# Optimization experiments

Hardware: AMD Instinct MI355X
Metric: run time of the kernel (lower is better)

Reference implementation:

```python
import jax, jax.numpy as jnp
import numpy as np

N = 50000
E = 800000
D = 128


def setup_inputs() -> dict:
    key = jax.random.key(0)
    ks = jax.random.split(key, 10)
    x = jax.random.normal(ks[0], (N, D), dtype=jnp.float32)
    edge_index = jax.random.randint(ks[1], (2, E), 0, N, dtype=jnp.int32)
    s = 1.0 / np.sqrt(D)
    W1 = jax.random.uniform(ks[2], (D, D), jnp.float32, -s, s)
    b1 = jnp.zeros((D,), jnp.float32)
    W2 = jax.random.uniform(ks[3], (D, D), jnp.float32, -s, s)
    b2 = jnp.zeros((D,), jnp.float32)
    Wt = jax.random.uniform(ks[4], (D, 1), jnp.float32, -s, s)
    bt = jnp.zeros((1,), jnp.float32)
    We = jax.random.uniform(ks[5], (D, 1), jnp.float32, -s, s)
    be = jnp.zeros((1,), jnp.float32)
    return {"x": x, "edge_index": edge_index, "W1": W1, "b1": b1,
            "W2": W2, "b2": b2, "Wt": Wt, "bt": bt, "We": We, "be": be}


def _gcn_norm(edge_index, n):
    # add self-loops, then symmetric normalization D^-1/2 (A+I) D^-1/2
    loop = jnp.arange(n, dtype=edge_index.dtype)
    src = jnp.concatenate([edge_index[0], loop])
    dst = jnp.concatenate([edge_index[1], loop])
    ones = jnp.ones(src.shape[0], dtype=jnp.float32)
    deg = jax.ops.segment_sum(ones, dst, num_segments=n)
    dinv = jnp.where(deg > 0, jax.lax.rsqrt(deg), 0.0)
    norm = dinv[src] * dinv[dst]  # [E+N]
    return src, dst, norm


def _gcn_conv(h, W, b, src, dst, norm, n):
    h = h @ W                                   # [N, D'] dense GEMM
    msg = h[src] * norm[:, None]                # gather + scale
    out = jax.ops.segment_sum(msg, dst, num_segments=n)  # scatter-add
    return out + b


def reference(x, edge_index, W1, b1, W2, b2, Wt, bt, We, be):
    n = x.shape[0]
    src, dst, norm = _gcn_norm(edge_index, n)
    h = jax.nn.relu(_gcn_conv(x, W1, b1, src, dst, norm, n))
    h = jax.nn.relu(_gcn_conv(h, W2, b2, src, dst, norm, n))
    # dropout is identity at inference (eval mode)
    survival_time = h @ Wt + bt   # [N, 1]
    event_status = h @ We + be    # [N, 1]
    return survival_time, event_status
```

## Files before the change

kernel.cpp:

```cpp
#include <hip/hip_runtime.h>
#include <hip/hip_fp16.h>
#include <math.h>

#define NN 50000
#define NE 800000
#define DD 128

#define NB  196
#define CAP 5300
#define EPB 4096

#define CONV_B 6250

typedef _Float16 half8_t __attribute__((ext_vector_type(8)));
typedef float f32x4 __attribute__((ext_vector_type(4)));


__global__ __launch_bounds__(256) void k_init_bcur(int* __restrict__ bcur) {
    int t = threadIdx.x;
    if (t < NB) bcur[t] = t * CAP;
}

__global__ __launch_bounds__(256) void k_phaseA(const int* __restrict__ src, const int* __restrict__ dst,
                                                int* __restrict__ bcur, unsigned int* __restrict__ ebuf) {
    __shared__ int hist[256];
    __shared__ int scanbuf[256];
    __shared__ int gbase[256];
    __shared__ unsigned int stage[EPB];
    __shared__ int tgt[EPB];

    const int tid = threadIdx.x;
    const int e0  = blockIdx.x * EPB;
    int nE = NE - e0; if (nE > EPB) nE = EPB;

    hist[tid] = 0;
    __syncthreads();

    unsigned int pk[16];
    unsigned int br[16];
    #pragma unroll
    for (int j = 0; j < 16; ++j) {
        int idx = tid + j * 256;
        if (idx < nE) {
            int e = e0 + idx;
            int s = src[e], d = dst[e];
            int b = d >> 8;
            int r = atomicAdd(&hist[b], 1);
            pk[j] = (unsigned int)s | ((unsigned int)(d & 255) << 16);
            br[j] = (unsigned int)b | ((unsigned int)r << 8);
        }
    }
    __syncthreads();
    int v = hist[tid];
    scanbuf[tid] = v;
    __syncthreads();
    for (int o = 1; o < 256; o <<= 1) {
        int t2 = (tid >= o) ? scanbuf[tid - o] : 0;
        __syncthreads();
        scanbuf[tid] += t2;
        __syncthreads();
    }
    int base_excl = scanbuf[tid] - v;
    if (tid < NB && v > 0) gbase[tid] = atomicAdd(&bcur[tid], v);
    hist[tid] = base_excl;
    __syncthreads();

    #pragma unroll
    for (int j = 0; j < 16; ++j) {
        int idx = tid + j * 256;
        if (idx < nE) {
            int b = br[j] & 255;
            int r = (int)(br[j] >> 8);
            int pos = hist[b] + r;
            stage[pos] = pk[j];
            tgt[pos]   = gbase[b] + r;
        }
    }
    __syncthreads();
    #pragma unroll
    for (int j = 0; j < 16; ++j) {
        int idx = tid + j * 256;
        if (idx < nE) ebuf[tgt[idx]] = stage[idx];
    }
}

__global__ __launch_bounds__(256) void k_bucket_scan(const int* __restrict__ bcur, int* __restrict__ bbase,
                                                     int* __restrict__ row_ptr) {
    __shared__ int s[256];
    int tid = threadIdx.x;
    int sz = (tid < NB) ? (bcur[tid] - tid * CAP) : 0;
    s[tid] = sz;
    __syncthreads();
    for (int o = 1; o < 256; o <<= 1) {
        int t = (tid >= o) ? s[tid - o] : 0;
        __syncthreads();
        s[tid] += t;
        __syncthreads();
    }
    if (tid < NB) bbase[tid] = s[tid] - sz;
    if (tid == 0) row_ptr[NN] = NE;
}

__global__ __launch_bounds__(256) void k_build_csr(const unsigned int* __restrict__ ebuf,
                                                   const int* __restrict__ bcur,
                                                   const int* __restrict__ bbase,
                                                   int* __restrict__ row_ptr,
                                                   float* __restrict__ dinv,
                                                   unsigned short* __restrict__ col) {
    __shared__ int cnt[256];
    __shared__ int scanb[256];
    __shared__ unsigned short stage[CAP];

    const int b   = blockIdx.x;
    const int tid = threadIdx.x;
    const int seg0 = b * CAP;
    const int sb   = bcur[b] - seg0;
    const int n0   = b << 8;
    int nb = NN - n0; if (nb > 256) nb = 256;

    cnt[tid] = 0;
    __syncthreads();
    for (int p = tid; p < sb; p += 256) {
        unsigned int e = ebuf[seg0 + p];
        atomicAdd(&cnt[(e >> 16) & 255], 1);
    }
    __syncthreads();
    int v = cnt[tid];
    scanb[tid] = v;
    __syncthreads();
    for (int o = 1; o < 256; o <<= 1) {
        int t = (tid >= o) ? scanb[tid - o] : 0;
        __syncthreads();
        scanb[tid] += t;
        __syncthreads();
    }
    int excl = scanb[tid] - v;
    const int rbase = bbase[b];
    if (tid < nb) {
        row_ptr[n0 + tid] = rbase + excl;
        dinv[n0 + tid] = rsqrtf(1.0f + (float)v);
    }
    cnt[tid] = excl;
    __syncthreads();
    for (int p = tid; p < sb; p += 256) {
        unsigned int e = ebuf[seg0 + p];
        int pos = atomicAdd(&cnt[(e >> 16) & 255], 1);
        stage[pos] = (unsigned short)(e & 0xFFFFu);
    }
    __syncthreads();
    for (int p = tid; p < sb; p += 256) {
        col[rbase + p] = stage[p];
    }
}


__global__ __launch_bounds__(256) void k_prep(const float* __restrict__ x,
                                              const float* __restrict__ W1, const float* __restrict__ W2,
                                              __half* __restrict__ Xh,
                                              __half* __restrict__ WT1, __half* __restrict__ WT2) {
    int b = blockIdx.x;
    int tid = threadIdx.x;
    if (b < CONV_B) {
        int idx = b * 256 + tid;
        if (idx < (NN * DD) / 4) {
            float4 v = ((const float4*)x)[idx];
            __half2 a = __floats2half2_rn(v.x, v.y);
            __half2 c = __floats2half2_rn(v.z, v.w);
            uint2 pk;
            pk.x = *(unsigned int*)&a;
            pk.y = *(unsigned int*)&c;
            ((uint2*)Xh)[idx] = pk;
        }
    } else {
        const float* W  = (b == CONV_B) ? W1 : W2;
        __half*      WT = (b == CONV_B) ? WT1 : WT2;
        int n = tid >> 1;
        int k0 = (tid & 1) * 64;
        #pragma unroll 8
        for (int j = 0; j < 64; ++j) {
            int k = k0 + j;
            WT[n * DD + k] = __float2half(W[k * DD + n]);
        }
    }
}


#define LPAD 136

__global__ __launch_bounds__(256) void k_gemm_mfma(const __half* __restrict__ Xh, const __half* __restrict__ WT,
                                                   const float* __restrict__ dinv, __half* __restrict__ G) {
    __shared__ __half Wl[DD * LPAD];
    __shared__ __half Al[64 * LPAD];

    const int tid  = threadIdx.x;
    const int row0 = blockIdx.x * 64;

    {
        const uint4* WTg = (const uint4*)WT;
        #pragma unroll
        for (int j = 0; j < 8; ++j) {
            int u = tid + j * 256;
            int n = u >> 4, koff = (u & 15) * 8;
            uint4 v = WTg[u];
            *(uint4*)&Wl[n * LPAD + koff] = v;
        }
    }
    {
        #pragma unroll
        for (int j = 0; j < 4; ++j) {
            int u = tid + j * 256;
            int r = u >> 4, koff = (u & 15) * 8;
            uint4 v;
            if (row0 + r < NN) v = *(const uint4*)&Xh[(size_t)(row0 + r) * DD + koff];
            else { v.x = 0; v.y = 0; v.z = 0; v.w = 0; }
            *(uint4*)&Al[r * LPAD + koff] = v;
        }
    }
    __syncthreads();

    const int wave = tid >> 6;
    const int lane = tid & 63;
    const int m    = lane & 15;
    const int quad = lane >> 4;

    f32x4 acc[8];
    #pragma unroll
    for (int t = 0; t < 8; ++t) acc[t] = (f32x4){0.f, 0.f, 0.f, 0.f};

    #pragma unroll
    for (int kk = 0; kk < DD; kk += 32) {
        half8_t a = *(const half8_t*)&Al[(wave * 16 + m) * LPAD + kk + quad * 8];
        #pragma unroll
        for (int t = 0; t < 8; ++t) {
            half8_t b = *(const half8_t*)&Wl[(t * 16 + m) * LPAD + kk + quad * 8];
            acc[t] = __builtin_amdgcn_mfma_f32_16x16x32_f16(a, b, acc[t], 0, 0, 0);
        }
    }

    __syncthreads();

    float4 dv = *(const float4*)&dinv[row0 + wave * 16 + quad * 4];

    #pragma unroll
    for (int t = 0; t < 8; ++t) {
        #pragma unroll
        for (int r = 0; r < 4; ++r) {
            int row_l = wave * 16 + quad * 4 + r;
            int c     = t * 16 + m;
            float val = acc[t][r] * ((const float*)&dv)[r];
            Al[row_l * LPAD + c] = __float2half(val);
        }
    }
    __syncthreads();

    {
        #pragma unroll
        for (int j = 0; j < 4; ++j) {
            int u = tid + j * 256;
            int r = u >> 4, koff = (u & 15) * 8;
            if (row0 + r < NN) {
                uint4 v = *(const uint4*)&Al[r * LPAD + koff];
                *(uint4*)&G[(size_t)(row0 + r) * DD + koff] = v;
            }
        }
    }
}


__device__ inline float4 h4_to_f4(uint2 r) {
    __half2 a = *(__half2*)&r.x;
    __half2 b = *(__half2*)&r.y;
    float2 lo = __half22float2(a), hi = __half22float2(b);
    return make_float4(lo.x, lo.y, hi.x, hi.y);
}

__device__ inline uint2 f4_to_h4(float4 v) {
    __half2 a = __floats2half2_rn(v.x, v.y);
    __half2 b = __floats2half2_rn(v.z, v.w);
    uint2 r;
    r.x = *(unsigned int*)&a;
    r.y = *(unsigned int*)&b;
    return r;
}

__device__ inline float4 gather_node4(const __half* __restrict__ G, int node, int lane,
                                      const unsigned short* __restrict__ col, int beg, int end) {
    const int hs = lane >> 5;
    const int fo = lane & 31;
    const size_t foff = (size_t)fo * 4;

    float4 accA, accB = make_float4(0.f, 0.f, 0.f, 0.f);
    {
        float4 v = h4_to_f4(*(const uint2*)(G + (size_t)node * DD + foff));
        accA = (hs == 0) ? v : make_float4(0.f, 0.f, 0.f, 0.f);
    }

    int p = beg;
    for (; p + 3 < end; p += 4) {
        int sA = col[p + hs];
        int sB = col[p + 2 + hs];
        float4 vA = h4_to_f4(*(const uint2*)(G + (size_t)sA * DD + foff));
        float4 vB = h4_to_f4(*(const uint2*)(G + (size_t)sB * DD + foff));
        accA.x += vA.x; accA.y += vA.y; accA.z += vA.z; accA.w += vA.w;
        accB.x += vB.x; accB.y += vB.y; accB.z += vB.z; accB.w += vB.w;
    }
    for (; p < end; p += 2) {
        int idx = p + hs;
        bool active = (hs == 0) || (p + 1 < end);
        if (idx >= end) idx = p;
        int s = col[idx];
        float4 v = h4_to_f4(*(const uint2*)(G + (size_t)s * DD + foff));
        if (active) {
            accA.x += v.x; accA.y += v.y; accA.z += v.z; accA.w += v.w;
        }
    }
    accA.x += accB.x; accA.y += accB.y; accA.z += accB.z; accA.w += accB.w;
    accA.x += __shfl_xor(accA.x, 32, 64);
    accA.y += __shfl_xor(accA.y, 32, 64);
    accA.z += __shfl_xor(accA.z, 32, 64);
    accA.w += __shfl_xor(accA.w, 32, 64);
    return accA;
}

__global__ __launch_bounds__(256) void k_aggregate(const __half* __restrict__ G, const float* __restrict__ dinv,
                                                   const int* __restrict__ row_ptr, const unsigned short* __restrict__ col,
                                                   const float* __restrict__ bias, __half* __restrict__ H) {
    int node = blockIdx.x * 4 + (threadIdx.x >> 6);
    if (node >= NN) return;
    int lane = threadIdx.x & 63;

    int beg = row_ptr[node];
    int end = row_ptr[node + 1];
    float4 acc = gather_node4(G, node, lane, col, beg, end);

    float di = dinv[node];
    int fo = lane & 31;
    float4 bv = ((const float4*)bias)[fo];
    float4 hv;
    hv.x = fmaxf(fmaf(di, acc.x, bv.x), 0.f);
    hv.y = fmaxf(fmaf(di, acc.y, bv.y), 0.f);
    hv.z = fmaxf(fmaf(di, acc.z, bv.z), 0.f);
    hv.w = fmaxf(fmaf(di, acc.w, bv.w), 0.f);
    if ((lane >> 5) == 0) {
        *(uint2*)(H + (size_t)node * DD + (size_t)fo * 4) = f4_to_h4(hv);
    }
}

__global__ __launch_bounds__(256) void k_aggregate_heads(const __half* __restrict__ G, const float* __restrict__ dinv,
                                                         const int* __restrict__ row_ptr, const unsigned short* __restrict__ col,
                                                         const float* __restrict__ bias,
                                                         const float* __restrict__ Wt, const float* __restrict__ bt,
                                                         const float* __restrict__ We, const float* __restrict__ be,
                                                         float* __restrict__ out) {
    int node = blockIdx.x * 4 + (threadIdx.x >> 6);
    if (node >= NN) return;
    int lane = threadIdx.x & 63;

    int beg = row_ptr[node];
    int end = row_ptr[node + 1];
    float4 acc = gather_node4(G, node, lane, col, beg, end);

    float di = dinv[node];
    int fo = lane & 31;
    float4 bv = ((const float4*)bias)[fo];
    float hx = fmaxf(fmaf(di, acc.x, bv.x), 0.f);
    float hy = fmaxf(fmaf(di, acc.y, bv.y), 0.f);
    float hz = fmaxf(fmaf(di, acc.z, bv.z), 0.f);
    float hw = fmaxf(fmaf(di, acc.w, bv.w), 0.f);

    float4 wt = ((const float4*)Wt)[fo];
    float4 we = ((const float4*)We)[fo];
    float t  = hx * wt.x + hy * wt.y + hz * wt.z + hw * wt.w;
    float ev = hx * we.x + hy * we.y + hz * we.z + hw * we.w;
    #pragma unroll
    for (int o = 16; o > 0; o >>= 1) {
        t  += __shfl_xor(t, o, 64);
        ev += __shfl_xor(ev, o, 64);
    }
    if (lane == 0) {
        out[node]      = t + bt[0];
        out[NN + node] = ev + be[0];
    }
}


extern "C" void kernel_launch(void* const* d_in, const int* in_sizes, int n_in,
                              void* d_out, int out_size, void* d_ws, size_t ws_size,
                              hipStream_t stream) {
    const float* x  = (const float*)d_in[0];
    const int*   ei = (const int*)d_in[1];
    const float* W1 = (const float*)d_in[2];
    const float* b1 = (const float*)d_in[3];
    const float* W2 = (const float*)d_in[4];
    const float* b2 = (const float*)d_in[5];
    const float* Wt = (const float*)d_in[6];
    const float* bt = (const float*)d_in[7];
    const float* We = (const float*)d_in[8];
    const float* be = (const float*)d_in[9];
    float* out = (float*)d_out;

    const int* srcI = ei;
    const int* dstI = ei + NE;

    char* w = (char*)d_ws;
    __half*         Xh    = (__half*)w;         w += (size_t)NN * DD * sizeof(__half);
    __half*         Gh    = (__half*)w;         w += (size_t)NN * DD * sizeof(__half);
    __half*         H1h   = (__half*)w;         w += (size_t)NN * DD * sizeof(__half);
    __half*         WT1   = (__half*)w;         w += (size_t)DD * DD * sizeof(__half);
    __half*         WT2   = (__half*)w;         w += (size_t)DD * DD * sizeof(__half);
    unsigned int*   ebuf  = (unsigned int*)w;   w += (size_t)NB * CAP * sizeof(unsigned int);
    unsigned short* col   = (unsigned short*)w; w += (size_t)NE * sizeof(unsigned short);
    float*          dinv  = (float*)w;          w += (size_t)(NN + 64) * sizeof(float);
    int*            rowp  = (int*)w;            w += (size_t)(NN + 1) * sizeof(int);
    int*            bcur  = (int*)w;            w += (size_t)NB * sizeof(int);
    int*            bbase = (int*)w;            w += (size_t)NB * sizeof(int);

    const int A_B    = (NE + EPB - 1) / EPB;
    const int AGG_B  = (NN + 3) / 4;
    const int GEMM_B = (NN + 63) / 64;

    hipLaunchKernelGGL(k_init_bcur,  dim3(1),          dim3(256), 0, stream, bcur);
    hipLaunchKernelGGL(k_phaseA,     dim3(A_B),        dim3(256), 0, stream, srcI, dstI, bcur, ebuf);
    hipLaunchKernelGGL(k_bucket_scan,dim3(1),          dim3(256), 0, stream, bcur, bbase, rowp);
    hipLaunchKernelGGL(k_build_csr,  dim3(NB),         dim3(256), 0, stream, ebuf, bcur, bbase, rowp, dinv, col);
    hipLaunchKernelGGL(k_prep,       dim3(CONV_B + 2), dim3(256), 0, stream, x, W1, W2, Xh, WT1, WT2);

    hipLaunchKernelGGL(k_gemm_mfma, dim3(GEMM_B), dim3(256), 0, stream, Xh, WT1, dinv, Gh);
    hipLaunchKernelGGL(k_aggregate, dim3(AGG_B),  dim3(256), 0, stream, Gh, dinv, rowp, col, b1, H1h);

    hipLaunchKernelGGL(k_gemm_mfma,       dim3(GEMM_B), dim3(256), 0, stream, H1h, WT2, dinv, Gh);
    hipLaunchKernelGGL(k_aggregate_heads, dim3(AGG_B),  dim3(256), 0, stream, Gh, dinv, rowp, col, b2,
                       Wt, bt, We, be, out);
}
```

Baseline: 223.4 us.

## Split node features into 32-column slabs for cache-local aggregation

Stores the fp16 feature matrices as four column slabs of 32 features each (per-slab rows of 64 bytes), so each aggregation block gathers from a single slab that is a quarter of the size, improving L2 locality for the random neighbor gathers. The aggregation kernels assign 8 lanes per neighbor and 8 edges in parallel per wave, interleaving chunk blocks so adjacent blocks share node groups. The head outputs are now combined across chunks with atomics, which needs a memset of the output. The separate bucket-scan kernel is folded into the CSR build, with each block redoing the scan, which removes one launch. The trade-offs are four times as many aggregation blocks, extra shuffle reductions and the output atomics.

Result: slower. 294.4 us (+31.8%).

```diff
diff --git a/kernel.cpp b/kernel.cpp
--- a/kernel.cpp
+++ b/kernel.cpp
@@ -11,6 +11,8 @@
 #define EPB 4096
 
 #define CONV_B 6250
+
+#define SLAB (NN * 32)
 
 typedef _Float16 half8_t __attribute__((ext_vector_type(8)));
 typedef float f32x4 __attribute__((ext_vector_type(4)));
@@ -84,26 +86,8 @@
     }
 }
 
-__global__ __launch_bounds__(256) void k_bucket_scan(const int* __restrict__ bcur, int* __restrict__ bbase,
-                                                     int* __restrict__ row_ptr) {
-    __shared__ int s[256];
-    int tid = threadIdx.x;
-    int sz = (tid < NB) ? (bcur[tid] - tid * CAP) : 0;
-    s[tid] = sz;
-    __syncthreads();
-    for (int o = 1; o < 256; o <<= 1) {
-        int t = (tid >= o) ? s[tid - o] : 0;
-        __syncthreads();
-        s[tid] += t;
-        __syncthreads();
-    }
-    if (tid < NB) bbase[tid] = s[tid] - sz;
-    if (tid == 0) row_ptr[NN] = NE;
-}
-
 __global__ __launch_bounds__(256) void k_build_csr(const unsigned int* __restrict__ ebuf,
                                                    const int* __restrict__ bcur,
-                                                   const int* __restrict__ bbase,
                                                    int* __restrict__ row_ptr,
                                                    float* __restrict__ dinv,
                                                    unsigned short* __restrict__ col) {
@@ -118,6 +102,18 @@
     const int n0   = b << 8;
     int nb = NN - n0; if (nb > 256) nb = 256;
 
+    int sz_t = (tid < NB) ? (bcur[tid] - tid * CAP) : 0;
+    scanb[tid] = sz_t;
+    __syncthreads();
+    for (int o = 1; o < 256; o <<= 1) {
+        int t = (tid >= o) ? scanb[tid - o] : 0;
+        __syncthreads();
+        scanb[tid] += t;
+        __syncthreads();
+    }
+    const int rbase = scanb[b] - sb;
+    __syncthreads();
+
     cnt[tid] = 0;
     __syncthreads();
     for (int p = tid; p < sb; p += 256) {
@@ -135,11 +131,11 @@
         __syncthreads();
     }
     int excl = scanb[tid] - v;
-    const int rbase = bbase[b];
     if (tid < nb) {
         row_ptr[n0 + tid] = rbase + excl;
         dinv[n0 + tid] = rsqrtf(1.0f + (float)v);
     }
+    if (b == 0 && tid == 0) row_ptr[NN] = NE;
     cnt[tid] = excl;
     __syncthreads();
     for (int p = tid; p < sb; p += 256) {
@@ -169,7 +165,10 @@
             uint2 pk;
             pk.x = *(unsigned int*)&a;
             pk.y = *(unsigned int*)&c;
-            ((uint2*)Xh)[idx] = pk;
+            int row = idx >> 5;
+            int c16 = idx & 31;
+            int ch = c16 >> 3, wi = c16 & 7;
+            *(uint2*)(Xh + (size_t)ch * SLAB + (size_t)row * 32 + wi * 4) = pk;
         }
     } else {
         const float* W  = (b == CONV_B) ? W1 : W2;
@@ -187,8 +186,8 @@
 
 #define LPAD 136
 
-__global__ __launch_bounds__(256) void k_gemm_mfma(const __half* __restrict__ Xh, const __half* __restrict__ WT,
-                                                   const float* __restrict__ dinv, __half* __restrict__ G) {
+__global__ __launch_bounds__(256) void k_gemm_mfma(const __half* __restrict__ Xc, const __half* __restrict__ WT,
+                                                   const float* __restrict__ dinv, __half* __restrict__ Gc) {
     __shared__ __half Wl[DD * LPAD];
     __shared__ __half Al[64 * LPAD];
 
@@ -209,11 +208,13 @@
         #pragma unroll
         for (int j = 0; j < 4; ++j) {
             int u = tid + j * 256;
-            int r = u >> 4, koff = (u & 15) * 8;
+            int r = u >> 4, c16 = u & 15;
+            int ch = c16 >> 2, wi = c16 & 3;
+            int grow = row0 + r;
             uint4 v;
-            if (row0 + r < NN) v = *(const uint4*)&Xh[(size_t)(row0 + r) * DD + koff];
+            if (grow < NN) v = *(const uint4*)(Xc + (size_t)ch * SLAB + (size_t)grow * 32 + wi * 8);
             else { v.x = 0; v.y = 0; v.z = 0; v.w = 0; }
-            *(uint4*)&Al[r * LPAD + koff] = v;
+            *(uint4*)&Al[r * LPAD + c16 * 8] = v;
         }
     }
     __syncthreads();
@@ -257,10 +258,12 @@
         #pragma unroll
         for (int j = 0; j < 4; ++j) {
             int u = tid + j * 256;
-            int r = u >> 4, koff = (u & 15) * 8;
-            if (row0 + r < NN) {
-                uint4 v = *(const uint4*)&Al[r * LPAD + koff];
-                *(uint4*)&G[(size_t)(row0 + r) * DD + koff] = v;
+            int r = u >> 4, c16 = u & 15;
+            int ch = c16 >> 2, wi = c16 & 3;
+            int grow = row0 + r;
+            if (grow < NN) {
+                uint4 v = *(const uint4*)&Al[r * LPAD + c16 * 8];
+                *(uint4*)(Gc + (size_t)ch * SLAB + (size_t)grow * 32 + wi * 8) = v;
             }
         }
     }
@@ -283,103 +286,109 @@
     return r;
 }
 
-__device__ inline float4 gather_node4(const __half* __restrict__ G, int node, int lane,
+__device__ inline float4 gather_chunk(const __half* __restrict__ slab, int node, int es, int fq,
                                       const unsigned short* __restrict__ col, int beg, int end) {
-    const int hs = lane >> 5;
-    const int fo = lane & 31;
-    const size_t foff = (size_t)fo * 4;
-
-    float4 accA, accB = make_float4(0.f, 0.f, 0.f, 0.f);
-    {
-        float4 v = h4_to_f4(*(const uint2*)(G + (size_t)node * DD + foff));
-        accA = (hs == 0) ? v : make_float4(0.f, 0.f, 0.f, 0.f);
-    }
+    float4 acc = make_float4(0.f, 0.f, 0.f, 0.f);
+    if (es == 0) acc = h4_to_f4(*(const uint2*)(slab + (size_t)node * 32 + fq * 4));
 
     int p = beg;
-    for (; p + 3 < end; p += 4) {
-        int sA = col[p + hs];
-        int sB = col[p + 2 + hs];
-        float4 vA = h4_to_f4(*(const uint2*)(G + (size_t)sA * DD + foff));
-        float4 vB = h4_to_f4(*(const uint2*)(G + (size_t)sB * DD + foff));
-        accA.x += vA.x; accA.y += vA.y; accA.z += vA.z; accA.w += vA.w;
-        accB.x += vB.x; accB.y += vB.y; accB.z += vB.z; accB.w += vB.w;
-    }
-    for (; p < end; p += 2) {
-        int idx = p + hs;
-        bool active = (hs == 0) || (p + 1 < end);
-        if (idx >= end) idx = p;
-        int s = col[idx];
-        float4 v = h4_to_f4(*(const uint2*)(G + (size_t)s * DD + foff));
-        if (active) {
-            accA.x += v.x; accA.y += v.y; accA.z += v.z; accA.w += v.w;
-        }
-    }
-    accA.x += accB.x; accA.y += accB.y; accA.z += accB.z; accA.w += accB.w;
-    accA.x += __shfl_xor(accA.x, 32, 64);
-    accA.y += __shfl_xor(accA.y, 32, 64);
-    accA.z += __shfl_xor(accA.z, 32, 64);
-    accA.w += __shfl_xor(accA.w, 32, 64);
-    return accA;
-}
-
-__global__ __launch_bounds__(256) void k_aggregate(const __half* __restrict__ G, const float* __restrict__ dinv,
-                                                   const int* __restrict__ row_ptr, const unsigned short* __restrict__ col,
-                                                   const float* __restrict__ bias, __half* __restrict__ H) {
-    int node = blockIdx.x * 4 + (threadIdx.x >> 6);
-    if (node >= NN) return;
-    int lane = threadIdx.x & 63;
-
+    for (; p + 15 < end; p += 16) {
+        int s0 = col[p + es];
+        int s1 = col[p + 8 + es];
+        float4 v0 = h4_to_f4(*(const uint2*)(slab + (size_t)s0 * 32 + fq * 4));
+        float4 v1 = h4_to_f4(*(const uint2*)(slab + (size_t)s1 * 32 + fq * 4));
+        acc.x += v0.x + v1.x; acc.y += v0.y + v1.y;
+        acc.z += v0.z + v1.z; acc.w += v0.w + v1.w;
+    }
+    for (; p < end; p += 8) {
+        int idx = p + es;
+        if (idx < end) {
+            int s0 = col[idx];
+            float4 v0 = h4_to_f4(*(const uint2*)(slab + (size_t)s0 * 32 + fq * 4));
+            acc.x += v0.x; acc.y += v0.y; acc.z += v0.z; acc.w += v0.w;
+        }
+    }
+    #pragma unroll
+    for (int o = 8; o < 64; o <<= 1) {
+        acc.x += __shfl_xor(acc.x, o, 64);
+        acc.y += __shfl_xor(acc.y, o, 64);
+        acc.z += __shfl_xor(acc.z, o, 64);
+        acc.w += __shfl_xor(acc.w, o, 64);
+    }
+    return acc;
+}
+
+__global__ __launch_bounds__(256) void k_aggregate_c(const __half* __restrict__ G, const float* __restrict__ dinv,
+                                                     const int* __restrict__ row_ptr, const unsigned short* __restrict__ col,
+                                                     const float* __restrict__ bias, __half* __restrict__ H) {
+    const int bx   = blockIdx.x;
+    const int slot = bx & 7;
+    const int chunk = slot >> 1;
+    const int ngrp  = (bx >> 3) * 2 + (slot & 1);
+    const int node  = ngrp * 4 + (threadIdx.x >> 6);
+    const int lane  = threadIdx.x & 63;
+    const int es = lane >> 3;
+    const int fq = lane & 7;
+
+    const __half* slab = G + (size_t)chunk * SLAB;
     int beg = row_ptr[node];
     int end = row_ptr[node + 1];
-    float4 acc = gather_node4(G, node, lane, col, beg, end);
-
-    float di = dinv[node];
-    int fo = lane & 31;
-    float4 bv = ((const float4*)bias)[fo];
-    float4 hv;
-    hv.x = fmaxf(fmaf(di, acc.x, bv.x), 0.f);
-    hv.y = fmaxf(fmaf(di, acc.y, bv.y), 0.f);
-    hv.z = fmaxf(fmaf(di, acc.z, bv.z), 0.f);
-    hv.w = fmaxf(fmaf(di, acc.w, bv.w), 0.f);
-    if ((lane >> 5) == 0) {
-        *(uint2*)(H + (size_t)node * DD + (size_t)fo * 4) = f4_to_h4(hv);
-    }
-}
-
-__global__ __launch_bounds__(256) void k_aggregate_heads(const __half* __restrict__ G, const float* __restrict__ dinv,
-                                                         const int* __restrict__ row_ptr, const unsigned short* __restrict__ col,
-                                                         const float* __restrict__ bias,
-                                                         const float* __restrict__ Wt, const float* __restrict__ bt,
-                                                         const float* __restrict__ We, const float* __restrict__ be,
-                                                         float* __restrict__ out) {
-    int node = blockIdx.x * 4 + (threadIdx.x >> 6);
-    if (node >= NN) return;
-    int lane = threadIdx.x & 63;
-
+    float4 acc = gather_chunk(slab, node, es, fq, col, beg, end);
+
+    if (es == 0) {
+        float di = dinv[node];
+        float4 bv = *(const float4*)(bias + chunk * 32 + fq * 4);
+        float4 hv;
+        hv.x = fmaxf(fmaf(di, acc.x, bv.x), 0.f);
+        hv.y = fmaxf(fmaf(di, acc.y, bv.y), 0.f);
+        hv.z = fmaxf(fmaf(di, acc.z, bv.z), 0.f);
+        hv.w = fmaxf(fmaf(di, acc.w, bv.w), 0.f);
+        *(uint2*)(H + (size_t)chunk * SLAB + (size_t)node * 32 + fq * 4) = f4_to_h4(hv);
+    }
+}
+
+__global__ __launch_bounds__(256) void k_aggregate_heads_c(const __half* __restrict__ G, const float* __restrict__ dinv,
+                                                           const int* __restrict__ row_ptr, const unsigned short* __restrict__ col,
+                                                           const float* __restrict__ bias,
+                                                           const float* __restrict__ Wt, const float* __restrict__ bt,
+                                                           const float* __restrict__ We, const float* __restrict__ be,
+                                                           float* __restrict__ out) {
+    const int bx   = blockIdx.x;
+    const int slot = bx & 7;
+    const int chunk = slot >> 1;
+    const int ngrp  = (bx >> 3) * 2 + (slot & 1);
+    const int node  = ngrp * 4 + (threadIdx.x >> 6);
+    const int lane  = threadIdx.x & 63;
+    const int es = lane >> 3;
+    const int fq = lane & 7;
+
+    const __half* slab = G + (size_t)chunk * SLAB;
     int beg = row_ptr[node];
     int end = row_ptr[node + 1];
-    float4 acc = gather_node4(G, node, lane, col, beg, end);
-
-    float di = dinv[node];
-    int fo = lane & 31;
-    float4 bv = ((const float4*)bias)[fo];
-    float hx = fmaxf(fmaf(di, acc.x, bv.x), 0.f);
-    float hy = fmaxf(fmaf(di, acc.y, bv.y), 0.f);
-    float hz = fmaxf(fmaf(di, acc.z, bv.z), 0.f);
-    float hw = fmaxf(fmaf(di, acc.w, bv.w), 0.f);
-
-    float4 wt = ((const float4*)Wt)[fo];
-    float4 we = ((const float4*)We)[fo];
-    float t  = hx * wt.x + hy * wt.y + hz * wt.z + hw * wt.w;
-    float ev = hx * we.x + hy * we.y + hz * we.z + hw * we.w;
-    #pragma unroll
-    for (int o = 16; o > 0; o >>= 1) {
-        t  += __shfl_xor(t, o, 64);
-        ev += __shfl_xor(ev, o, 64);
-    }
-    if (lane == 0) {
-        out[node]      = t + bt[0];
-        out[NN + node] = ev + be[0];
+    float4 acc = gather_chunk(slab, node, es, fq, col, beg, end);
+
+    if (es == 0) {
+        float di = dinv[node];
+        float4 bv = *(const float4*)(bias + chunk * 32 + fq * 4);
+        float hx = fmaxf(fmaf(di, acc.x, bv.x), 0.f);
+        float hy = fmaxf(fmaf(di, acc.y, bv.y), 0.f);
+        float hz = fmaxf(fmaf(di, acc.z, bv.z), 0.f);
+        float hw = fmaxf(fmaf(di, acc.w, bv.w), 0.f);
+
+        float4 wt = *(const float4*)(Wt + chunk * 32 + fq * 4);
+        float4 we = *(const float4*)(We + chunk * 32 + fq * 4);
+        float t  = hx * wt.x + hy * wt.y + hz * wt.z + hw * wt.w;
+        float ev = hx * we.x + hy * we.y + hz * we.z + hw * we.w;
+        #pragma unroll
+        for (int o = 1; o < 8; o <<= 1) {
+            t  += __shfl_xor(t, o, 64);
+            ev += __shfl_xor(ev, o, 64);
+        }
+        if (fq == 0) {
+            if (chunk == 0) { t += bt[0]; ev += be[0]; }
+            atomicAdd(&out[node], t);
+            atomicAdd(&out[NN + node], ev);
+        }
     }
 }
 
@@ -413,22 +422,22 @@
     float*          dinv  = (float*)w;          w += (size_t)(NN + 64) * sizeof(float);
     int*            rowp  = (int*)w;            w += (size_t)(NN + 1) * sizeof(int);
     int*            bcur  = (int*)w;            w += (size_t)NB * sizeof(int);
-    int*            bbase = (int*)w;            w += (size_t)NB * sizeof(int);
 
     const int A_B    = (NE + EPB - 1) / EPB;
-    const int AGG_B  = (NN + 3) / 4;
+    const int AGG_B  = (NN / 4) * 4;
     const int GEMM_B = (NN + 63) / 64;
+
+    hipMemsetAsync(out, 0, (size_t)out_size * sizeof(float), stream);
 
     hipLaunchKernelGGL(k_init_bcur,  dim3(1),          dim3(256), 0, stream, bcur);
     hipLaunchKernelGGL(k_phaseA,     dim3(A_B),        dim3(256), 0, stream, srcI, dstI, bcur, ebuf);
-    hipLaunchKernelGGL(k_bucket_scan,dim3(1),          dim3(256), 0, stream, bcur, bbase, rowp);
-    hipLaunchKernelGGL(k_build_csr,  dim3(NB),         dim3(256), 0, stream, ebuf, bcur, bbase, rowp, dinv, col);
+    hipLaunchKernelGGL(k_build_csr,  dim3(NB),         dim3(256), 0, stream, ebuf, bcur, rowp, dinv, col);
     hipLaunchKernelGGL(k_prep,       dim3(CONV_B + 2), dim3(256), 0, stream, x, W1, W2, Xh, WT1, WT2);
 
-    hipLaunchKernelGGL(k_gemm_mfma, dim3(GEMM_B), dim3(256), 0, stream, Xh, WT1, dinv, Gh);
-    hipLaunchKernelGGL(k_aggregate, dim3(AGG_B),  dim3(256), 0, stream, Gh, dinv, rowp, col, b1, H1h);
-
-    hipLaunchKernelGGL(k_gemm_mfma,       dim3(GEMM_B), dim3(256), 0, stream, H1h, WT2, dinv, Gh);
-    hipLaunchKernelGGL(k_aggregate_heads, dim3(AGG_B),  dim3(256), 0, stream, Gh, dinv, rowp, col, b2,
+    hipLaunchKernelGGL(k_gemm_mfma,   dim3(GEMM_B), dim3(256), 0, stream, Xh, WT1, dinv, Gh);
+    hipLaunchKernelGGL(k_aggregate_c, dim3(AGG_B),  dim3(256), 0, stream, Gh, dinv, rowp, col, b1, H1h);
+
+    hipLaunchKernelGGL(k_gemm_mfma,         dim3(GEMM_B), dim3(256), 0, stream, H1h, WT2, dinv, Gh);
+    hipLaunchKernelGGL(k_aggregate_heads_c, dim3(AGG_B),  dim3(256), 0, stream, Gh, dinv, rowp, col, b2,
                        Wt, bt, We, be, out);
 }
```
